# Optimization experiments

Measured on AMD Instinct MI355X. Metric: run time of the kernel, lower is better.

Reference implementation:

```python
import jax, jax.numpy as jnp
import numpy as np

B, CHANS, SAMPLES = 256, 22, 1125
DEPTH, CD1, CD2, KT = 9, 24, 9, 75
K_CHEB, N_CHEB_LAYERS, AVEPOOL = 3, 5, 5
W1 = SAMPLES - KT + 1          # 1051 after valid (1,75) conv
WP = W1 // AVEPOOL             # 210 after avgpool
FEAT = CD2 * WP                # 1890 -> fc1


def _bn(x, p, eps=1e-5):
    # eval-mode BatchNorm2d over channel axis 1; p rows = [gamma, beta, mean, var]
    g, b, m, v = p
    s = (1, -1, 1, 1)
    return (x - m.reshape(s)) / jnp.sqrt(v.reshape(s) + eps) * g.reshape(s) + b.reshape(s)


def _normalize_A(A, lmax=2.0):
    A = jax.nn.relu(A)
    n = A.shape[0]
    I = jnp.eye(n, dtype=A.dtype)
    A = A * (1.0 - I)            # zero diagonal
    A = A + A.T                  # symmetrize
    d = jnp.sum(A, axis=1)
    dis = 1.0 / jnp.sqrt(d + 1e-10)
    L = I - dis[:, None] * A * dis[None, :]
    return 2.0 * L / lmax - I


def _forward(x, channel_weight, tconv1_w, bn1, tconv2_w, bn2, da_w, da_b,
             cconv1_w, bn3, A, A_mask, cheby_W, cheby_b, cconv2_w, bn4,
             fc1_w, fc1_b, mlp_w1, mlp_b1, mlp_w2, mlp_b2):
    dn = ('NCHW', 'OIHW', 'NCHW')
    # lead weighting: (B,1,C,S) x (H,1,C) -> (B,H,C,S)
    x = jnp.einsum('bdcw,hdc->bhcw', x, channel_weight)
    # time_conv: pointwise 1x1 + BN + depthwise (1,KT) + BN + GELU
    x = jnp.einsum('bicw,oi->bocw', x, tconv1_w)
    x = _bn(x, bn1)
    x = jax.lax.conv_general_dilated(x, tconv2_w.reshape(CD1, 1, 1, KT), (1, 1),
                                     'VALID', feature_group_count=CD1,
                                     dimension_numbers=dn)
    x = jax.nn.gelu(_bn(x, bn2), approximate=False)
    # EEGDepthAttention: avg over chans, (7,1) conv on depth axis, softmax over depth
    xp = jnp.mean(x, axis=2, keepdims=True)        # (B,CD1,1,W1)
    xt = jnp.swapaxes(xp, 1, 2)                    # (B,1,CD1,W1)
    y = jax.lax.conv_general_dilated(xt, da_w.reshape(1, 1, 7, 1), (1, 1),
                                     ((3, 3), (0, 0)), dimension_numbers=dn)
    y = jax.nn.softmax(y + da_b.reshape(1, 1, 1, 1), axis=-2)
    x = jnp.swapaxes(y, 1, 2) * CHANS * x          # (B,CD1,C,W1)
    # channel conv part1: 1x1 + BN -> (B,CD2,C,W1)
    x = _bn(jnp.einsum('bicw,oi->bocw', x, cconv1_w), bn3)
    # normalized Laplacian from pruned learnable adjacency
    L = _normalize_A(A * jax.nn.sigmoid(A_mask))
    I = jnp.eye(CHANS, dtype=L.dtype)
    adjs = [I, L, 2.0 * (L @ L) - I][:K_CHEB]      # Chebyshev T_0..T_2
    b_, f_, c_, w_ = x.shape
    xr = jnp.transpose(x, (0, 3, 1, 2)).reshape(b_ * w_, f_, c_)  # (N,F,C)
    for l in range(N_CHEB_LAYERS):
        out = jnp.zeros_like(xr)
        for k in range(K_CHEB):
            out = out + jnp.einsum('cd,nfd,fo->noc', adjs[k], xr, cheby_W[l, k]) \
                      + cheby_b[l, k][None, :, None]
        xr = jax.nn.relu(out)
    x = jnp.transpose(xr.reshape(b_, w_, f_, c_), (0, 2, 3, 1))   # (B,CD2,C,W1)
    # channel conv part2: depthwise (CHANS,1) + BN + GELU -> (B,CD2,1,W1)
    x = jnp.einsum('bfcw,fc->bfw', x, cconv2_w)[:, :, None, :]
    x = jax.nn.gelu(_bn(x, bn4), approximate=False)
    # avgpool kernel/stride AVEPOOL on time; dropout is identity at eval
    x = x[..., :WP * AVEPOOL].reshape(b_, CD2, 1, WP, AVEPOOL).mean(-1)
    x = x.reshape(b_, -1)                           # (B,FEAT)
    x = x @ fc1_w + fc1_b                           # (B,5)
    x = jax.nn.elu(x @ mlp_w1 + mlp_b1) @ mlp_w2 + mlp_b2
    return jax.nn.softmax(x, axis=1)


def setup_inputs() -> dict:
    key = jax.random.key(0)
    ks = iter(jax.random.split(key, 40))

    def randn(shape, s=1.0):
        return jax.random.normal(next(ks), shape, jnp.float32) * s

    def bn_p(c):
        return jnp.stack([jax.random.uniform(next(ks), (c,)) * 0.5 + 0.75,
                          randn((c,), 0.1), randn((c,), 0.1),
                          jax.random.uniform(next(ks), (c,)) * 0.5 + 0.75])

    return {
        'x': randn((B, 1, CHANS, SAMPLES)),
        'channel_weight': randn((DEPTH, 1, CHANS), 0.3),
        'tconv1_w': randn((CD1, DEPTH), 0.3),
        'bn1': bn_p(CD1),
        'tconv2_w': randn((CD1, KT), 0.1),
        'bn2': bn_p(CD1),
        'da_w': randn((7,), 0.3),
        'da_b': randn((1,), 0.1),
        'cconv1_w': randn((CD2, CD1), 0.2),
        'bn3': bn_p(CD2),
        'A': jax.random.uniform(next(ks), (CHANS, CHANS)) * 0.49 + 0.01,
        'A_mask': jnp.ones((CHANS, CHANS), jnp.float32),
        'cheby_W': randn((N_CHEB_LAYERS, K_CHEB, CD2, CD2), 0.3),
        'cheby_b': jnp.zeros((N_CHEB_LAYERS, K_CHEB, CD2), jnp.float32),
        'cconv2_w': randn((CD2, CHANS), 0.2),
        'bn4': bn_p(CD2),
        'fc1_w': randn((FEAT, 5), 0.02),
        'fc1_b': jnp.zeros((5,), jnp.float32),
        'mlp_w1': randn((5, 64), 0.3),
        'mlp_b1': jnp.zeros((64,), jnp.float32),
        'mlp_w2': randn((64, 4), 0.2),
        'mlp_b2': jnp.zeros((4,), jnp.float32),
    }


def reference(x, channel_weight, tconv1_w, bn1, tconv2_w, bn2, da_w, da_b,
              cconv1_w, bn3, A, A_mask, cheby_W, cheby_b, cconv2_w, bn4,
              fc1_w, fc1_b, mlp_w1, mlp_b1, mlp_w2, mlp_b2):
    return _forward(x, channel_weight, tconv1_w, bn1, tconv2_w, bn2, da_w, da_b,
                    cconv1_w, bn3, A, A_mask, cheby_W, cheby_b, cconv2_w, bn4,
                    fc1_w, fc1_b, mlp_w1, mlp_b1, mlp_w2, mlp_b2)
```

## Files before the change

### kernel.cpp

```cpp
#include <hip/hip_runtime.h>
#include <hip/hip_bf16.h>
#include <math.h>

#define B_      256
#define CHANS   22
#define SAMPLES 1125
#define DEPTH   9
#define CD1     24
#define CD2     9
#define KT      75
#define W1      1051
#define WP      210
#define FEAT    1890
#define TW      11
#define NT      96

#define WS_D    528
#define WS_CC1  552
#define WS_B3   768
#define WS_L1   777
#define WS_L2   1261
#define WS_CC2  1745
#define WS_B4   1943
#define WS_BL   1952
#define WS_W2T  2000
#define WS_KTB  2528
#define WS_Z    4096

typedef short short8 __attribute__((ext_vector_type(8)));
typedef float f32x4  __attribute__((ext_vector_type(4)));

__device__ __forceinline__ float gelu_fast(float v) {
    float u = v * 0.70710678118654752f;
    float s = fabsf(u);
    float t = __builtin_amdgcn_rcpf(fmaf(0.3275911f, s, 1.0f));
    float p = fmaf(fmaf(fmaf(fmaf(1.061405429f, t, -1.453152027f), t,
                             1.421413741f), t, -0.284496736f), t, 0.254829592f) * t;
    float e = __builtin_amdgcn_exp2f(s * s * -1.4426950408889634f);
    float er = copysignf(fmaf(-p, e, 1.0f), u);
    return fmaf(0.5f * v, er, 0.5f * v);
}

__global__ __launch_bounds__(256) void precompute_kernel(
    const float* __restrict__ cw, const float* __restrict__ t1w,
    const float* __restrict__ bn1, const float* __restrict__ t2w,
    const float* __restrict__ bn2, const float* __restrict__ cc1w,
    const float* __restrict__ bn3, const float* __restrict__ A,
    const float* __restrict__ Am, const float* __restrict__ cbB,
    const float* __restrict__ cc2w, const float* __restrict__ bn4,
    float* __restrict__ ws)
{
    __shared__ float a1[CD1], a2[CD1];
    __shared__ float a3[CD2], a4[CD2];
    __shared__ float Ap[484], As[484], dis[22], L1s[484];
    const int tid = threadIdx.x;

    if (tid < CD1) {
        float g1 = bn1[tid], be1 = bn1[24 + tid], m1 = bn1[48 + tid], v1 = bn1[72 + tid];
        a1[tid] = g1 * rsqrtf(v1 + 1e-5f);
        float b1v = be1 - m1 * a1[tid];
        float g2 = bn2[tid], be2 = bn2[24 + tid], m2 = bn2[48 + tid], v2 = bn2[72 + tid];
        a2[tid] = g2 * rsqrtf(v2 + 1e-5f);
        float b2v = be2 - m2 * a2[tid];
        float S = 0.0f;
        for (int k = 0; k < KT; ++k) S += t2w[tid * KT + k];
        ws[WS_D + tid] = a2[tid] * b1v * S + b2v;
    }
    if (tid < CD2) {
        float g3 = bn3[tid], be3 = bn3[9 + tid], m3 = bn3[18 + tid], v3 = bn3[27 + tid];
        a3[tid] = g3 * rsqrtf(v3 + 1e-5f);
        ws[WS_B3 + tid] = be3 - m3 * a3[tid];
        float g4 = bn4[tid], be4 = bn4[9 + tid], m4 = bn4[18 + tid], v4 = bn4[27 + tid];
        a4[tid] = g4 * rsqrtf(v4 + 1e-5f);
        ws[WS_B4 + tid] = be4 - m4 * a4[tid];
    }
    __syncthreads();

    for (int e = tid; e < CHANS * 24; e += blockDim.x) {
        int c = e / 24, o = e - c * 24;
        float m = 0.0f;
        for (int h = 0; h < DEPTH; ++h) m += t1w[o * DEPTH + h] * cw[h * CHANS + c];
        ws[WS_W2T + e] = a2[o] * a1[o] * m;
    }
    {
        __hip_bfloat16* ktb = (__hip_bfloat16*)(ws + WS_KTB);
        for (int e = tid; e < 32 * 96; e += blockDim.x) {
            int o = e / 96, k = e - o * 96;
            float v = (o < CD1 && k < KT) ? t2w[o * KT + k] : 0.0f;
            ktb[e] = __float2bfloat16(v);
        }
    }
    for (int e = tid; e < CD2 * CD1; e += blockDim.x) {
        int o = e / CD1;
        ws[WS_CC1 + e] = a3[o] * cc1w[e] * 22.0f;
    }
    for (int e = tid; e < CD2 * CHANS; e += blockDim.x) {
        int f = e / CHANS;
        ws[WS_CC2 + e] = a4[f] * cc2w[e];
    }
    for (int e = tid; e < 45; e += blockDim.x) {
        int l = e / 9, o = e - l * 9;
        ws[WS_BL + e] = cbB[(l * 3 + 0) * 9 + o] + cbB[(l * 3 + 1) * 9 + o] + cbB[(l * 3 + 2) * 9 + o];
    }
    for (int e = tid; e < 484; e += blockDim.x) {
        int c = e / 22, d = e - c * 22;
        float v = A[e] / (1.0f + expf(-Am[e]));
        v = fmaxf(v, 0.0f);
        if (c == d) v = 0.0f;
        Ap[e] = v;
    }
    __syncthreads();
    for (int e = tid; e < 484; e += blockDim.x) {
        int c = e / 22, d = e - c * 22;
        As[e] = Ap[e] + Ap[d * 22 + c];
    }
    __syncthreads();
    if (tid < 22) {
        float s = 0.0f;
        for (int d = 0; d < 22; ++d) s += As[tid * 22 + d];
        dis[tid] = rsqrtf(s + 1e-10f);
    }
    __syncthreads();
    for (int e = tid; e < 484; e += blockDim.x) {
        int c = e / 22, d = e - c * 22;
        float v = -dis[c] * As[e] * dis[d];
        L1s[e] = v;
        ws[WS_L1 + e] = v;
    }
    __syncthreads();
    for (int e = tid; e < 484; e += blockDim.x) {
        int c = e / 22, d = e - c * 22;
        float s = 0.0f;
        for (int k2 = 0; k2 < 22; ++k2) s += L1s[c * 22 + k2] * L1s[k2 * 22 + d];
        ws[WS_L2 + e] = 2.0f * s - (c == d ? 1.0f : 0.0f);
    }
}

#define OX   0
#define XSTR 268
#define OG   2948
#define GSTR 532
#define OS   8800
#define XP   9088
#define SMEM_F 9360

__global__ __launch_bounds__(256, 4) void main_kernel(
    const float* __restrict__ x, const float* __restrict__ t2w,
    const float* __restrict__ daw_g, const float* __restrict__ dab_g,
    const float* __restrict__ cbW, float* __restrict__ ws)
{
    __shared__ float sm[SMEM_F];
    const int tid = threadIdx.x;
    const int b = blockIdx.y;
    const int w0 = blockIdx.x * TW;
    const float* cst = ws;
    float* zbuf = ws + WS_Z;

    const int lane = tid & 63;
    const int wid  = tid >> 6;
    const int quad = lane >> 4;
    const int lt   = lane & 15;

    {
        __hip_bfloat16* xbuf = (__hip_bfloat16*)sm;
        for (int e = tid; e < 22 * 112; e += 256) {
            int ch = e / 112, j = e - ch * 112;
            int s = w0 + j;
            float v = (j < 85 && s < SAMPLES) ? x[(b * CHANS + ch) * SAMPLES + s] : 0.0f;
            __hip_bfloat16 h = __float2bfloat16(v);
            xbuf[e] = h;
            if (j > 0) xbuf[2464 + e - 1] = h;
            if (j == 111) xbuf[2464 + e] = __float2bfloat16(0.0f);
        }
    }
    __syncthreads();

    {
        short8 afr0[3], afr1[3];
        const short* ktb = (const short*)(cst + WS_KTB);
        #pragma unroll
        for (int kt = 0; kt < 3; ++kt) {
            afr0[kt] = *(const short8*)(ktb + lt * 96 + kt * 32 + quad * 8);
            afr1[kt] = *(const short8*)(ktb + (lt + 16) * 96 + kt * 32 + quad * 8);
        }
        const int xebase = (lt & 1) ? (2464 - 1 + lt) : lt;
        const int* smi = (const int*)sm;

        for (int c = wid; c < CHANS; c += 4) {
            f32x4 acc0 = {0.f, 0.f, 0.f, 0.f}, acc1 = {0.f, 0.f, 0.f, 0.f};
            #pragma unroll
            for (int kt = 0; kt < 3; ++kt) {
                int bi = (xebase + c * 112 + quad * 8 + kt * 32) >> 1;
                union { int i[4]; short8 s; } B;
                B.i[0] = smi[bi];     B.i[1] = smi[bi + 1];
                B.i[2] = smi[bi + 2]; B.i[3] = smi[bi + 3];
                acc0 = __builtin_amdgcn_mfma_f32_16x16x32_bf16(afr0[kt], B.s, acc0, 0, 0, 0);
                acc1 = __builtin_amdgcn_mfma_f32_16x16x32_bf16(afr1[kt], B.s, acc1, 0, 0, 0);
            }
            const int t = lt;
            if (t < TW) {
                {
                    const float* w2p = cst + WS_W2T + c * 24 + quad * 4;
                    const float* ddp = cst + WS_D + quad * 4;
                    float g0 = gelu_fast(fmaf(w2p[0], acc0[0], ddp[0]));
                    float g1 = gelu_fast(fmaf(w2p[1], acc0[1], ddp[1]));
                    float g2 = gelu_fast(fmaf(w2p[2], acc0[2], ddp[2]));
                    float g3 = gelu_fast(fmaf(w2p[3], acc0[3], ddp[3]));
                    *(float4*)&sm[OG + t * GSTR + c * 24 + quad * 4] = make_float4(g0, g1, g2, g3);
                }
                if (quad < 2) {
                    const float* w2p = cst + WS_W2T + c * 24 + 16 + quad * 4;
                    const float* ddp = cst + WS_D + 16 + quad * 4;
                    float g0 = gelu_fast(fmaf(w2p[0], acc1[0], ddp[0]));
                    float g1 = gelu_fast(fmaf(w2p[1], acc1[1], ddp[1]));
                    float g2 = gelu_fast(fmaf(w2p[2], acc1[2], ddp[2]));
                    float g3 = gelu_fast(fmaf(w2p[3], acc1[3], ddp[3]));
                    *(float4*)&sm[OG + t * GSTR + c * 24 + 16 + quad * 4] = make_float4(g0, g1, g2, g3);
                }
            }
        }
    }
    __syncthreads();

    for (int e = tid; e < CD1 * TW; e += 256) {
        int d = e / TW, tt = e - d * TW;
        float s = 0.0f;
        #pragma unroll
        for (int ch = 0; ch < CHANS; ++ch) s += sm[OG + tt * GSTR + ch * 24 + d];
        sm[XP + e] = s * (1.0f / 22.0f);
    }
    __syncthreads();
    for (int e = tid; e < CD1 * TW; e += 256) {
        int d = e / TW, tt = e - d * TW;
        float y = dab_g[0];
        #pragma unroll
        for (int j = 0; j < 7; ++j) {
            int dd = d + j - 3;
            if (dd >= 0 && dd < CD1) y += daw_g[j] * sm[XP + dd * TW + tt];
        }
        sm[OS + d * 12 + tt] = y;
    }
    __syncthreads();
    if (tid < TW) {
        float mx = -1e30f;
        for (int d = 0; d < CD1; ++d) mx = fmaxf(mx, sm[OS + d * 12 + tid]);
        float sum = 0.0f;
        for (int d = 0; d < CD1; ++d) {
            float e2 = expf(sm[OS + d * 12 + tid] - mx);
            sm[OS + d * 12 + tid] = e2;
            sum += e2;
        }
        float inv = 1.0f / sum;
        for (int d = 0; d < CD1; ++d) sm[OS + d * 12 + tid] *= inv;
    }
    __syncthreads();

    const int c = tid / TW;
    const int t = tid - c * TW;
    const bool act = (tid < 242);

    float xo[CD2];
    if (act) {
        float garr[CD1];
        {
            const float4* gp = (const float4*)&sm[OG + t * GSTR + c * 24];
            #pragma unroll
            for (int q = 0; q < 6; ++q) {
                float4 v = gp[q];
                garr[4 * q] = v.x; garr[4 * q + 1] = v.y;
                garr[4 * q + 2] = v.z; garr[4 * q + 3] = v.w;
            }
        }
        #pragma unroll
        for (int o = 0; o < CD2; ++o) xo[o] = cst[WS_B3 + o];
        #pragma unroll
        for (int i = 0; i < CD1; ++i) {
            float s = sm[OS + i * 12 + t];
            float p = s * garr[i];
            #pragma unroll
            for (int o = 0; o < CD2; ++o)
                xo[o] = fmaf(cst[WS_CC1 + o * CD1 + i], p, xo[o]);
        }
        float4* xp = (float4*)&sm[OX + t * XSTR + c * 12];
        xp[0] = make_float4(xo[0], xo[1], xo[2], xo[3]);
        xp[1] = make_float4(xo[4], xo[5], xo[6], xo[7]);
        xp[2] = make_float4(xo[8], 0.0f, 0.0f, 0.0f);
    }
    __syncthreads();

    float t1row[CHANS], t2row[CHANS];
    if (act) {
        #pragma unroll
        for (int d = 0; d < CHANS; ++d) {
            t1row[d] = cst[WS_L1 + c * 22 + d];
            t2row[d] = cst[WS_L2 + c * 22 + d];
        }
    }

    for (int l = 0; l < 5; ++l) {
        float y1[CD2], y2[CD2];
        if (act) {
            #pragma unroll
            for (int o = 0; o < CD2; ++o) { y1[o] = 0.0f; y2[o] = 0.0f; }
            #pragma unroll
            for (int d = 0; d < CHANS; ++d) {
                const float4* p = (const float4*)&sm[OX + t * XSTR + d * 12];
                float4 a = p[0], bb = p[1];
                float x8 = sm[OX + t * XSTR + d * 12 + 8];
                float w1c = t1row[d], w2c = t2row[d];
                y1[0] = fmaf(w1c, a.x, y1[0]);  y2[0] = fmaf(w2c, a.x, y2[0]);
                y1[1] = fmaf(w1c, a.y, y1[1]);  y2[1] = fmaf(w2c, a.y, y2[1]);
                y1[2] = fmaf(w1c, a.z, y1[2]);  y2[2] = fmaf(w2c, a.z, y2[2]);
                y1[3] = fmaf(w1c, a.w, y1[3]);  y2[3] = fmaf(w2c, a.w, y2[3]);
                y1[4] = fmaf(w1c, bb.x, y1[4]); y2[4] = fmaf(w2c, bb.x, y2[4]);
                y1[5] = fmaf(w1c, bb.y, y1[5]); y2[5] = fmaf(w2c, bb.y, y2[5]);
                y1[6] = fmaf(w1c, bb.z, y1[6]); y2[6] = fmaf(w2c, bb.z, y2[6]);
                y1[7] = fmaf(w1c, bb.w, y1[7]); y2[7] = fmaf(w2c, bb.w, y2[7]);
                y1[8] = fmaf(w1c, x8, y1[8]);   y2[8] = fmaf(w2c, x8, y2[8]);
            }
            float out[CD2];
            #pragma unroll
            for (int o = 0; o < CD2; ++o) out[o] = cst[WS_BL + l * 9 + o];
            #pragma unroll
            for (int f = 0; f < CD2; ++f) {
                const float* w0p = cbW + ((l * 3 + 0) * 9 + f) * 9;
                const float* w1p = cbW + ((l * 3 + 1) * 9 + f) * 9;
                const float* w2p = cbW + ((l * 3 + 2) * 9 + f) * 9;
                float xv = xo[f], yv1 = y1[f], yv2 = y2[f];
                #pragma unroll
                for (int o = 0; o < CD2; ++o)
                    out[o] = fmaf(w0p[o], xv, fmaf(w1p[o], yv1, fmaf(w2p[o], yv2, out[o])));
            }
            #pragma unroll
            for (int o = 0; o < CD2; ++o) xo[o] = fmaxf(out[o], 0.0f);
        }
        __syncthreads();
        if (act) {
            float4* xp = (float4*)&sm[OX + t * XSTR + c * 12];
            xp[0] = make_float4(xo[0], xo[1], xo[2], xo[3]);
            xp[1] = make_float4(xo[4], xo[5], xo[6], xo[7]);
            xp[2] = make_float4(xo[8], 0.0f, 0.0f, 0.0f);
        }
        __syncthreads();
    }

    if (tid < CD2 * TW) {
        int f = tid / TW, tt = tid - f * TW;
        float a = cst[WS_B4 + f];
        #pragma unroll
        for (int ch = 0; ch < CHANS; ++ch)
            a = fmaf(cst[WS_CC2 + f * CHANS + ch], sm[OX + tt * XSTR + ch * 12 + f], a);
        float z = gelu_fast(a);
        int w = w0 + tt;
        if (w < W1) zbuf[(b * CD2 + f) * W1 + w] = z;
    }
}

__global__ __launch_bounds__(256) void head_kernel(
    const float* __restrict__ ws, const float* __restrict__ fc1w,
    const float* __restrict__ fc1b, const float* __restrict__ w1,
    const float* __restrict__ b1, const float* __restrict__ w2,
    const float* __restrict__ b2, float* __restrict__ out)
{
    __shared__ float red[5][256];
    __shared__ float l5[5];
    __shared__ float hbuf[64];
    const int tid = threadIdx.x;
    const int b = blockIdx.x;
    const float* zb = ws + WS_Z + b * CD2 * W1;

    float part[5] = {0, 0, 0, 0, 0};
    for (int i = tid; i < FEAT; i += 256) {
        int f = i / WP, t = i - f * WP;
        const float* zp = zb + f * W1 + 5 * t;
        float pooled = 0.2f * (zp[0] + zp[1] + zp[2] + zp[3] + zp[4]);
        #pragma unroll
        for (int j = 0; j < 5; ++j) part[j] = fmaf(pooled, fc1w[i * 5 + j], part[j]);
    }
    #pragma unroll
    for (int j = 0; j < 5; ++j) red[j][tid] = part[j];
    __syncthreads();
    for (int ofs = 128; ofs > 0; ofs >>= 1) {
        if (tid < ofs) {
            #pragma unroll
            for (int j = 0; j < 5; ++j) red[j][tid] += red[j][tid + ofs];
        }
        __syncthreads();
    }
    if (tid < 5) l5[tid] = red[tid][0] + fc1b[tid];
    __syncthreads();
    if (tid < 64) {
        float a = b1[tid];
        #pragma unroll
        for (int j = 0; j < 5; ++j) a = fmaf(l5[j], w1[j * 64 + tid], a);
        hbuf[tid] = (a > 0.0f) ? a : expm1f(a);
    }
    __syncthreads();
    if (tid == 0) {
        float o4[4];
        #pragma unroll
        for (int m = 0; m < 4; ++m) {
            float a = b2[m];
            for (int k = 0; k < 64; ++k) a = fmaf(hbuf[k], w2[k * 4 + m], a);
            o4[m] = a;
        }
        float mx = fmaxf(fmaxf(o4[0], o4[1]), fmaxf(o4[2], o4[3]));
        float s = 0.0f;
        #pragma unroll
        for (int m = 0; m < 4; ++m) { o4[m] = expf(o4[m] - mx); s += o4[m]; }
        float inv = 1.0f / s;
        #pragma unroll
        for (int m = 0; m < 4; ++m) out[b * 4 + m] = o4[m] * inv;
    }
}

extern "C" void kernel_launch(void* const* d_in, const int* in_sizes, int n_in,
                              void* d_out, int out_size, void* d_ws, size_t ws_size,
                              hipStream_t stream)
{
    const float* x    = (const float*)d_in[0];
    const float* cw   = (const float*)d_in[1];
    const float* t1w  = (const float*)d_in[2];
    const float* bn1  = (const float*)d_in[3];
    const float* t2w  = (const float*)d_in[4];
    const float* bn2  = (const float*)d_in[5];
    const float* daw  = (const float*)d_in[6];
    const float* dab  = (const float*)d_in[7];
    const float* cc1w = (const float*)d_in[8];
    const float* bn3  = (const float*)d_in[9];
    const float* A    = (const float*)d_in[10];
    const float* Am   = (const float*)d_in[11];
    const float* cbW  = (const float*)d_in[12];
    const float* cbB  = (const float*)d_in[13];
    const float* cc2w = (const float*)d_in[14];
    const float* bn4  = (const float*)d_in[15];
    const float* fc1w = (const float*)d_in[16];
    const float* fc1b = (const float*)d_in[17];
    const float* w1   = (const float*)d_in[18];
    const float* b1   = (const float*)d_in[19];
    const float* w2   = (const float*)d_in[20];
    const float* b2   = (const float*)d_in[21];
    float* ws  = (float*)d_ws;
    float* out = (float*)d_out;

    hipLaunchKernelGGL(precompute_kernel, dim3(1), dim3(256), 0, stream,
                       cw, t1w, bn1, t2w, bn2, cc1w, bn3, A, Am, cbB, cc2w, bn4, ws);
    hipLaunchKernelGGL(main_kernel, dim3(NT, B_), dim3(256), 0, stream,
                       x, t2w, daw, dab, cbW, ws);
    hipLaunchKernelGGL(head_kernel, dim3(B_), dim3(256), 0, stream,
                       ws, fc1w, fc1b, w1, b1, w2, b2, out);
}
```

Baseline: 884.2 us.

## Run Chebyshev graph propagation on fp16 MFMA with hi/lo split precision

Replaces the scalar FMA loops that apply the Laplacian matrices L1 and L2 in each of the five Chebyshev layers with fp16 MFMA matrix multiplies. A hi/lo split of both operands, with a scaled low part, keeps close to fp32 accuracy. The temporal conv MFMA switches from bf16 to fp16, and the GELU activations are stored in shared memory as fp16, which shrinks the LDS footprint. The trade-off is extra packing and transpose traffic through shared memory and possible precision loss, since the hi*lo-only scheme drops the lo*lo term.

```diff
diff --git a/kernel.cpp b/kernel.cpp
--- a/kernel.cpp
+++ b/kernel.cpp
@@ -15,19 +15,21 @@
 #define TW      11
 #define NT      96
 
-#define WS_D    528
-#define WS_CC1  552
-#define WS_B3   768
-#define WS_L1   777
-#define WS_L2   1261
-#define WS_CC2  1745
-#define WS_B4   1943
-#define WS_BL   1952
-#define WS_W2T  2000
-#define WS_KTB  2528
-#define WS_Z    4096
-
-typedef short short8 __attribute__((ext_vector_type(8)));
+#define WS_D    0
+#define WS_CC1  24
+#define WS_B3   240
+#define WS_B4   249
+#define WS_BL   258
+#define WS_CC2  303
+#define WS_W2T  504
+#define WS_KTB  1032
+#define WS_T16  2568
+#define WS_Z    4992
+
+#define LOSCALE    4096.0f
+#define LOSCALE_I  2.44140625e-4f
+
+typedef _Float16 half8 __attribute__((ext_vector_type(8)));
 typedef float f32x4  __attribute__((ext_vector_type(4)));
 
 __device__ __forceinline__ float gelu_fast(float v) {
@@ -39,6 +41,13 @@
     float e = __builtin_amdgcn_exp2f(s * s * -1.4426950408889634f);
     float er = copysignf(fmaf(-p, e, 1.0f), u);
     return fmaf(0.5f * v, er, 0.5f * v);
+}
+
+__device__ __forceinline__ half8 ld_half8(const _Float16* p) {
+    union { uint2 u[2]; half8 h; } r;
+    r.u[0] = *(const uint2*)p;
+    r.u[1] = *(const uint2*)(p + 4);
+    return r.h;
 }
 
 __global__ __launch_bounds__(256) void precompute_kernel(
@@ -52,7 +61,7 @@
 {
     __shared__ float a1[CD1], a2[CD1];
     __shared__ float a3[CD2], a4[CD2];
-    __shared__ float Ap[484], As[484], dis[22], L1s[484];
+    __shared__ float Ap[484], As[484], dis[22], L1s[484], L2s[484];
     const int tid = threadIdx.x;
 
     if (tid < CD1) {
@@ -83,11 +92,11 @@
         ws[WS_W2T + e] = a2[o] * a1[o] * m;
     }
     {
-        __hip_bfloat16* ktb = (__hip_bfloat16*)(ws + WS_KTB);
+        _Float16* ktb = (_Float16*)(ws + WS_KTB);
         for (int e = tid; e < 32 * 96; e += blockDim.x) {
             int o = e / 96, k = e - o * 96;
             float v = (o < CD1 && k < KT) ? t2w[o * KT + k] : 0.0f;
-            ktb[e] = __float2bfloat16(v);
+            ktb[e] = (_Float16)v;
         }
     }
     for (int e = tid; e < CD2 * CD1; e += blockDim.x) {
@@ -123,33 +132,44 @@
     __syncthreads();
     for (int e = tid; e < 484; e += blockDim.x) {
         int c = e / 22, d = e - c * 22;
-        float v = -dis[c] * As[e] * dis[d];
-        L1s[e] = v;
-        ws[WS_L1 + e] = v;
+        L1s[e] = -dis[c] * As[e] * dis[d];
     }
     __syncthreads();
     for (int e = tid; e < 484; e += blockDim.x) {
         int c = e / 22, d = e - c * 22;
         float s = 0.0f;
         for (int k2 = 0; k2 < 22; ++k2) s += L1s[c * 22 + k2] * L1s[k2 * 22 + d];
-        ws[WS_L2 + e] = 2.0f * s - (c == d ? 1.0f : 0.0f);
+        L2s[e] = 2.0f * s - (c == d ? 1.0f : 0.0f);
+    }
+    __syncthreads();
+    {
+        _Float16* t16 = (_Float16*)(ws + WS_T16);
+        for (int e = tid; e < 4096; e += blockDim.x) {
+            int plane = e >> 11, rem = e & 2047;
+            int which = rem >> 10, r = (rem >> 5) & 31, d = rem & 31;
+            float v = 0.0f;
+            if (r < 22 && d < 22) v = which ? L2s[r * 22 + d] : L1s[r * 22 + d];
+            _Float16 hi = (_Float16)v;
+            t16[e] = plane ? (_Float16)((v - (float)hi) * LOSCALE) : hi;
+        }
     }
 }
 
-#define OX   0
-#define XSTR 268
-#define OG   2948
-#define GSTR 532
-#define OS   8800
-#define XP   9088
-#define SMEM_F 9360
+#define XA16H 0
+#define XA16L 4032
+#define OG16  8064
+#define YF    4032
+#define OSF   8388
+#define XPF   8676
+#define SMEM_F 8960
 
 __global__ __launch_bounds__(256, 4) void main_kernel(
-    const float* __restrict__ x, const float* __restrict__ t2w,
-    const float* __restrict__ daw_g, const float* __restrict__ dab_g,
-    const float* __restrict__ cbW, float* __restrict__ ws)
+    const float* __restrict__ x, const float* __restrict__ daw_g,
+    const float* __restrict__ dab_g, const float* __restrict__ cbW,
+    float* __restrict__ ws)
 {
     __shared__ float sm[SMEM_F];
+    _Float16* sm16 = (_Float16*)sm;
     const int tid = threadIdx.x;
     const int b = blockIdx.y;
     const int w0 = blockIdx.x * TW;
@@ -161,27 +181,24 @@
     const int quad = lane >> 4;
     const int lt   = lane & 15;
 
+    for (int e = tid; e < 22 * 112; e += 256) {
+        int ch = e / 112, j = e - ch * 112;
+        int s = w0 + j;
+        float v = (j < 85 && s < SAMPLES) ? x[(b * CHANS + ch) * SAMPLES + s] : 0.0f;
+        _Float16 h = (_Float16)v;
+        sm16[e] = h;
+        if (j > 0) sm16[2464 + e - 1] = h;
+        if (j == 111) sm16[2464 + e] = (_Float16)0.0f;
+    }
+    __syncthreads();
+
     {
-        __hip_bfloat16* xbuf = (__hip_bfloat16*)sm;
-        for (int e = tid; e < 22 * 112; e += 256) {
-            int ch = e / 112, j = e - ch * 112;
-            int s = w0 + j;
-            float v = (j < 85 && s < SAMPLES) ? x[(b * CHANS + ch) * SAMPLES + s] : 0.0f;
-            __hip_bfloat16 h = __float2bfloat16(v);
-            xbuf[e] = h;
-            if (j > 0) xbuf[2464 + e - 1] = h;
-            if (j == 111) xbuf[2464 + e] = __float2bfloat16(0.0f);
-        }
-    }
-    __syncthreads();
-
-    {
-        short8 afr0[3], afr1[3];
-        const short* ktb = (const short*)(cst + WS_KTB);
+        half8 afr0[3], afr1[3];
+        const _Float16* ktb = (const _Float16*)(cst + WS_KTB);
         #pragma unroll
         for (int kt = 0; kt < 3; ++kt) {
-            afr0[kt] = *(const short8*)(ktb + lt * 96 + kt * 32 + quad * 8);
-            afr1[kt] = *(const short8*)(ktb + (lt + 16) * 96 + kt * 32 + quad * 8);
+            afr0[kt] = *(const half8*)(ktb + lt * 96 + kt * 32 + quad * 8);
+            afr1[kt] = *(const half8*)(ktb + (lt + 16) * 96 + kt * 32 + quad * 8);
         }
         const int xebase = (lt & 1) ? (2464 - 1 + lt) : lt;
         const int* smi = (const int*)sm;
@@ -191,31 +208,33 @@
             #pragma unroll
             for (int kt = 0; kt < 3; ++kt) {
                 int bi = (xebase + c * 112 + quad * 8 + kt * 32) >> 1;
-                union { int i[4]; short8 s; } B;
+                union { int i[4]; half8 s; } B;
                 B.i[0] = smi[bi];     B.i[1] = smi[bi + 1];
                 B.i[2] = smi[bi + 2]; B.i[3] = smi[bi + 3];
-                acc0 = __builtin_amdgcn_mfma_f32_16x16x32_bf16(afr0[kt], B.s, acc0, 0, 0, 0);
-                acc1 = __builtin_amdgcn_mfma_f32_16x16x32_bf16(afr1[kt], B.s, acc1, 0, 0, 0);
+                acc0 = __builtin_amdgcn_mfma_f32_16x16x32_f16(afr0[kt], B.s, acc0, 0, 0, 0);
+                acc1 = __builtin_amdgcn_mfma_f32_16x16x32_f16(afr1[kt], B.s, acc1, 0, 0, 0);
             }
             const int t = lt;
             if (t < TW) {
                 {
                     const float* w2p = cst + WS_W2T + c * 24 + quad * 4;
                     const float* ddp = cst + WS_D + quad * 4;
-                    float g0 = gelu_fast(fmaf(w2p[0], acc0[0], ddp[0]));
-                    float g1 = gelu_fast(fmaf(w2p[1], acc0[1], ddp[1]));
-                    float g2 = gelu_fast(fmaf(w2p[2], acc0[2], ddp[2]));
-                    float g3 = gelu_fast(fmaf(w2p[3], acc0[3], ddp[3]));
-                    *(float4*)&sm[OG + t * GSTR + c * 24 + quad * 4] = make_float4(g0, g1, g2, g3);
+                    union { _Float16 h[4]; uint2 v; } pk;
+                    pk.h[0] = (_Float16)gelu_fast(fmaf(w2p[0], acc0[0], ddp[0]));
+                    pk.h[1] = (_Float16)gelu_fast(fmaf(w2p[1], acc0[1], ddp[1]));
+                    pk.h[2] = (_Float16)gelu_fast(fmaf(w2p[2], acc0[2], ddp[2]));
+                    pk.h[3] = (_Float16)gelu_fast(fmaf(w2p[3], acc0[3], ddp[3]));
+                    *(uint2*)&sm16[OG16 + t * 532 + c * 24 + quad * 4] = pk.v;
                 }
                 if (quad < 2) {
                     const float* w2p = cst + WS_W2T + c * 24 + 16 + quad * 4;
                     const float* ddp = cst + WS_D + 16 + quad * 4;
-                    float g0 = gelu_fast(fmaf(w2p[0], acc1[0], ddp[0]));
-                    float g1 = gelu_fast(fmaf(w2p[1], acc1[1], ddp[1]));
-                    float g2 = gelu_fast(fmaf(w2p[2], acc1[2], ddp[2]));
-                    float g3 = gelu_fast(fmaf(w2p[3], acc1[3], ddp[3]));
-                    *(float4*)&sm[OG + t * GSTR + c * 24 + 16 + quad * 4] = make_float4(g0, g1, g2, g3);
+                    union { _Float16 h[4]; uint2 v; } pk;
+                    pk.h[0] = (_Float16)gelu_fast(fmaf(w2p[0], acc1[0], ddp[0]));
+                    pk.h[1] = (_Float16)gelu_fast(fmaf(w2p[1], acc1[1], ddp[1]));
+                    pk.h[2] = (_Float16)gelu_fast(fmaf(w2p[2], acc1[2], ddp[2]));
+                    pk.h[3] = (_Float16)gelu_fast(fmaf(w2p[3], acc1[3], ddp[3]));
+                    *(uint2*)&sm16[OG16 + t * 532 + c * 24 + 16 + quad * 4] = pk.v;
                 }
             }
         }
@@ -226,8 +245,8 @@
         int d = e / TW, tt = e - d * TW;
         float s = 0.0f;
         #pragma unroll
-        for (int ch = 0; ch < CHANS; ++ch) s += sm[OG + tt * GSTR + ch * 24 + d];
-        sm[XP + e] = s * (1.0f / 22.0f);
+        for (int ch = 0; ch < CHANS; ++ch) s += (float)sm16[OG16 + tt * 532 + ch * 24 + d];
+        sm[XPF + e] = s * (1.0f / 22.0f);
     }
     __syncthreads();
     for (int e = tid; e < CD1 * TW; e += 256) {
@@ -236,87 +255,120 @@
         #pragma unroll
         for (int j = 0; j < 7; ++j) {
             int dd = d + j - 3;
-            if (dd >= 0 && dd < CD1) y += daw_g[j] * sm[XP + dd * TW + tt];
-        }
-        sm[OS + d * 12 + tt] = y;
+            if (dd >= 0 && dd < CD1) y += daw_g[j] * sm[XPF + dd * TW + tt];
+        }
+        sm[OSF + d * 12 + tt] = y;
     }
     __syncthreads();
     if (tid < TW) {
         float mx = -1e30f;
-        for (int d = 0; d < CD1; ++d) mx = fmaxf(mx, sm[OS + d * 12 + tid]);
+        for (int d = 0; d < CD1; ++d) mx = fmaxf(mx, sm[OSF + d * 12 + tid]);
         float sum = 0.0f;
         for (int d = 0; d < CD1; ++d) {
-            float e2 = expf(sm[OS + d * 12 + tid] - mx);
-            sm[OS + d * 12 + tid] = e2;
+            float e2 = expf(sm[OSF + d * 12 + tid] - mx);
+            sm[OSF + d * 12 + tid] = e2;
             sum += e2;
         }
         float inv = 1.0f / sum;
-        for (int d = 0; d < CD1; ++d) sm[OS + d * 12 + tid] *= inv;
-    }
-    __syncthreads();
-
-    const int c = tid / TW;
-    const int t = tid - c * TW;
+        for (int d = 0; d < CD1; ++d) sm[OSF + d * 12 + tid] *= inv;
+    }
+    __syncthreads();
+
+    const int c4 = tid / TW;
+    const int t4 = tid - c4 * TW;
     const bool act = (tid < 242);
+
+    for (int e = tid; e < 1120; e += 256) {
+        int row = e / 10, d = 22 + (e - row * 10);
+        sm16[XA16H + row * 36 + d] = (_Float16)0.0f;
+        sm16[XA16L + row * 36 + d] = (_Float16)0.0f;
+    }
+    for (int e = tid; e < 286; e += 256) {
+        int row = 99 + e / 22, d = e - 22 * (e / 22);
+        sm16[XA16H + row * 36 + d] = (_Float16)0.0f;
+        sm16[XA16L + row * 36 + d] = (_Float16)0.0f;
+    }
 
     float xo[CD2];
     if (act) {
         float garr[CD1];
         {
-            const float4* gp = (const float4*)&sm[OG + t * GSTR + c * 24];
-            #pragma unroll
-            for (int q = 0; q < 6; ++q) {
-                float4 v = gp[q];
-                garr[4 * q] = v.x; garr[4 * q + 1] = v.y;
-                garr[4 * q + 2] = v.z; garr[4 * q + 3] = v.w;
-            }
+            union { uint u[12]; _Float16 h[24]; } gg;
+            const uint* gsrc = (const uint*)&sm16[OG16 + t4 * 532 + c4 * 24];
+            #pragma unroll
+            for (int q = 0; q < 12; ++q) gg.u[q] = gsrc[q];
+            #pragma unroll
+            for (int i = 0; i < 24; ++i) garr[i] = (float)gg.h[i];
         }
         #pragma unroll
         for (int o = 0; o < CD2; ++o) xo[o] = cst[WS_B3 + o];
         #pragma unroll
         for (int i = 0; i < CD1; ++i) {
-            float s = sm[OS + i * 12 + t];
+            float s = sm[OSF + i * 12 + t4];
             float p = s * garr[i];
             #pragma unroll
             for (int o = 0; o < CD2; ++o)
                 xo[o] = fmaf(cst[WS_CC1 + o * CD1 + i], p, xo[o]);
         }
-        float4* xp = (float4*)&sm[OX + t * XSTR + c * 12];
-        xp[0] = make_float4(xo[0], xo[1], xo[2], xo[3]);
-        xp[1] = make_float4(xo[4], xo[5], xo[6], xo[7]);
-        xp[2] = make_float4(xo[8], 0.0f, 0.0f, 0.0f);
-    }
-    __syncthreads();
-
-    float t1row[CHANS], t2row[CHANS];
-    if (act) {
-        #pragma unroll
-        for (int d = 0; d < CHANS; ++d) {
-            t1row[d] = cst[WS_L1 + c * 22 + d];
-            t2row[d] = cst[WS_L2 + c * 22 + d];
-        }
-    }
-
+        #pragma unroll
+        for (int f = 0; f < 9; ++f) {
+            float v = xo[f];
+            _Float16 hi = (_Float16)v;
+            _Float16 lo = (_Float16)((v - (float)hi) * LOSCALE);
+            int row = (t4 * 9 + f) * 36 + c4;
+            sm16[XA16H + row] = hi;
+            sm16[XA16L + row] = lo;
+        }
+    }
+    __syncthreads();
+
+    const int Tsel = wid >> 1;
+    const int ccG1 = (wid & 1) * 16 + lt;
+    const _Float16* t16 = (const _Float16*)(cst + WS_T16);
+    const half8 bT_hi = *(const half8*)(t16 + Tsel * 1024 + ccG1 * 32 + quad * 8);
+    const half8 bT_lo = *(const half8*)(t16 + 2048 + Tsel * 1024 + ccG1 * 32 + quad * 8);
+    const f32x4 zz = {0.f, 0.f, 0.f, 0.f};
+
+    #pragma unroll 1
     for (int l = 0; l < 5; ++l) {
-        float y1[CD2], y2[CD2];
+        f32x4 y[7];
+        #pragma unroll
+        for (int mt = 0; mt < 7; ++mt) {
+            half8 ah = ld_half8(&sm16[XA16H + (mt * 16 + lt) * 36 + quad * 8]);
+            half8 al = ld_half8(&sm16[XA16L + (mt * 16 + lt) * 36 + quad * 8]);
+            f32x4 ahi = __builtin_amdgcn_mfma_f32_16x16x32_f16(ah, bT_hi, zz, 0, 0, 0);
+            f32x4 alo = __builtin_amdgcn_mfma_f32_16x16x32_f16(al, bT_hi, zz, 0, 0, 0);
+            alo = __builtin_amdgcn_mfma_f32_16x16x32_f16(ah, bT_lo, alo, 0, 0, 0);
+            f32x4 yv;
+            #pragma unroll
+            for (int r = 0; r < 4; ++r) yv[r] = fmaf(alo[r], LOSCALE_I, ahi[r]);
+            y[mt] = yv;
+        }
+        if (ccG1 < 22) {
+            const int cb = ccG1 * 11;
+            #pragma unroll
+            for (int mt = 0; mt < 7; ++mt) {
+                int m0 = mt * 16 + quad * 4;
+                if (m0 < 99) {
+                    int t0 = (m0 * 57) >> 9;
+                    int f0 = m0 - 9 * t0;
+                    #pragma unroll
+                    for (int r = 0; r < 4; ++r) {
+                        if (m0 + r < 99)
+                            sm[YF + (Tsel * 9 + f0) * 242 + cb + t0] = y[mt][r];
+                        ++f0; if (f0 == 9) { f0 = 0; ++t0; }
+                    }
+                }
+            }
+        }
+        __syncthreads();
+
         if (act) {
-            #pragma unroll
-            for (int o = 0; o < CD2; ++o) { y1[o] = 0.0f; y2[o] = 0.0f; }
-            #pragma unroll
-            for (int d = 0; d < CHANS; ++d) {
-                const float4* p = (const float4*)&sm[OX + t * XSTR + d * 12];
-                float4 a = p[0], bb = p[1];
-                float x8 = sm[OX + t * XSTR + d * 12 + 8];
-                float w1c = t1row[d], w2c = t2row[d];
-                y1[0] = fmaf(w1c, a.x, y1[0]);  y2[0] = fmaf(w2c, a.x, y2[0]);
-                y1[1] = fmaf(w1c, a.y, y1[1]);  y2[1] = fmaf(w2c, a.y, y2[1]);
-                y1[2] = fmaf(w1c, a.z, y1[2]);  y2[2] = fmaf(w2c, a.z, y2[2]);
-                y1[3] = fmaf(w1c, a.w, y1[3]);  y2[3] = fmaf(w2c, a.w, y2[3]);
-                y1[4] = fmaf(w1c, bb.x, y1[4]); y2[4] = fmaf(w2c, bb.x, y2[4]);
-                y1[5] = fmaf(w1c, bb.y, y1[5]); y2[5] = fmaf(w2c, bb.y, y2[5]);
-                y1[6] = fmaf(w1c, bb.z, y1[6]); y2[6] = fmaf(w2c, bb.z, y2[6]);
-                y1[7] = fmaf(w1c, bb.w, y1[7]); y2[7] = fmaf(w2c, bb.w, y2[7]);
-                y1[8] = fmaf(w1c, x8, y1[8]);   y2[8] = fmaf(w2c, x8, y2[8]);
+            float y1v[CD2], y2v[CD2];
+            #pragma unroll
+            for (int f = 0; f < 9; ++f) {
+                y1v[f] = sm[YF + f * 242 + tid];
+                y2v[f] = sm[YF + (9 + f) * 242 + tid];
             }
             float out[CD2];
             #pragma unroll
@@ -326,30 +378,40 @@
                 const float* w0p = cbW + ((l * 3 + 0) * 9 + f) * 9;
                 const float* w1p = cbW + ((l * 3 + 1) * 9 + f) * 9;
                 const float* w2p = cbW + ((l * 3 + 2) * 9 + f) * 9;
-                float xv = xo[f], yv1 = y1[f], yv2 = y2[f];
+                float xv = xo[f], yv1 = y1v[f], yv2 = y2v[f];
                 #pragma unroll
                 for (int o = 0; o < CD2; ++o)
                     out[o] = fmaf(w0p[o], xv, fmaf(w1p[o], yv1, fmaf(w2p[o], yv2, out[o])));
             }
             #pragma unroll
             for (int o = 0; o < CD2; ++o) xo[o] = fmaxf(out[o], 0.0f);
+            if (l < 4) {
+                #pragma unroll
+                for (int f = 0; f < 9; ++f) {
+                    float v = xo[f];
+                    _Float16 hi = (_Float16)v;
+                    _Float16 lo = (_Float16)((v - (float)hi) * LOSCALE);
+                    int row = (t4 * 9 + f) * 36 + c4;
+                    sm16[XA16H + row] = hi;
+                    sm16[XA16L + row] = lo;
+                }
+            }
         }
         __syncthreads();
-        if (act) {
-            float4* xp = (float4*)&sm[OX + t * XSTR + c * 12];
-            xp[0] = make_float4(xo[0], xo[1], xo[2], xo[3]);
-            xp[1] = make_float4(xo[4], xo[5], xo[6], xo[7]);
-            xp[2] = make_float4(xo[8], 0.0f, 0.0f, 0.0f);
-        }
-        __syncthreads();
-    }
+    }
+
+    if (act) {
+        #pragma unroll
+        for (int f = 0; f < 9; ++f) sm[YF + f * 242 + tid] = xo[f];
+    }
+    __syncthreads();
 
     if (tid < CD2 * TW) {
         int f = tid / TW, tt = tid - f * TW;
         float a = cst[WS_B4 + f];
         #pragma unroll
         for (int ch = 0; ch < CHANS; ++ch)
-            a = fmaf(cst[WS_CC2 + f * CHANS + ch], sm[OX + tt * XSTR + ch * 12 + f], a);
+            a = fmaf(cst[WS_CC2 + f * CHANS + ch], sm[YF + f * 242 + ch * 11 + tt], a);
         float z = gelu_fast(a);
         int w = w0 + tt;
         if (w < W1) zbuf[(b * CD2 + f) * W1 + w] = z;
@@ -446,7 +508,7 @@
     hipLaunchKernelGGL(precompute_kernel, dim3(1), dim3(256), 0, stream,
                        cw, t1w, bn1, t2w, bn2, cc1w, bn3, A, Am, cbB, cc2w, bn4, ws);
     hipLaunchKernelGGL(main_kernel, dim3(NT, B_), dim3(256), 0, stream,
-                       x, t2w, daw, dab, cbW, ws);
+                       x, daw, dab, cbW, ws);
     hipLaunchKernelGGL(head_kernel, dim3(B_), dim3(256), 0, stream,
                        ws, fc1w, fc1b, w1, b1, w2, b2, out);
 }
```

New measurement: 864.7 us. -2.2%, faster.
